# Optimization experiments

Measured on AMD Instinct MI355X. Metric: run time of the kernel, lower is better.

Reference implementation:

```python
import jax, jax.numpy as jnp
import numpy as np

EPS = 1e-08
SLOPE = 0.01  # LeakyReLU default negative_slope
B = 2097152
H = 32

def leaky_relu(x):
    return jnp.where(x >= 0, x, SLOPE * x)

def gram_schmidt(v, w):
    # v, w: [b,3]
    v_on = v / (jnp.linalg.norm(v, axis=-1, keepdims=True) + EPS)
    proj = jnp.sum(w * v_on, axis=-1, keepdims=True) * v_on
    w_orth = w - proj
    w_on = w_orth / (jnp.linalg.norm(w_orth, axis=-1, keepdims=True) + EPS)
    u_on = jnp.cross(v_on, w_on)
    R = jnp.stack((v_on, w_on, u_on), axis=-1)  # [b,3,3]
    v_local = jnp.einsum('bji,bj->bi', R, v)    # R^T @ v
    w_local = jnp.einsum('bji,bj->bi', R, w)
    return R, v_local, w_local

def setup_inputs() -> dict:
    key = jax.random.key(0)
    ks = jax.random.split(key, 12)
    std = 0.0001  # init_weights() normal std
    return {
        'v': jax.random.normal(ks[0], (B, 3), jnp.float32),
        'w': jax.random.normal(ks[1], (B, 3), jnp.float32),
        'W1': jax.random.normal(ks[2], (H, 3), jnp.float32) * std,
        'b1': jax.random.normal(ks[3], (H,), jnp.float32) * std,
        'W2': jax.random.normal(ks[4], (H, H), jnp.float32) * std,
        'b2': jax.random.normal(ks[5], (H,), jnp.float32) * std,
        'Wd1': jax.random.normal(ks[6], (H, H), jnp.float32) * std,
        'bd1': jax.random.normal(ks[7], (H,), jnp.float32) * std,
        'Wd2': jax.random.normal(ks[8], (3, H), jnp.float32) * std,
        'bd2': jax.random.normal(ks[9], (3,), jnp.float32) * std,
        'bias': jnp.array([[0.0, 0.0, -9.81]], jnp.float32),
    }

def reference(v, w, W1, b1, W2, b2, Wd1, bd1, Wd2, bd2, bias):
    shapes = v.shape
    b = shapes[0]
    v = v.reshape(b, 3)
    w = w.reshape(b, 3)
    R, v_local, w_local = gram_schmidt(v, w)
    feat = jnp.concatenate([v_local[..., :1], w_local[..., :2]], axis=-1)  # [b,3]
    h1 = leaky_relu(feat @ W1.T + b1)           # [b,H]
    h = leaky_relu(h1 @ W2.T + b2) * h1         # [b,H]
    y = leaky_relu(h @ Wd1.T + bd1) @ Wd2.T + bd2  # [b,3]
    y = jnp.einsum('bij,bj->bi', R, y) + bias
    return y.reshape(shapes)
```

## Files before the change

### kernel.cpp

```cpp
#include <hip/hip_runtime.h>

typedef __attribute__((ext_vector_type(8))) short short8;
typedef __attribute__((ext_vector_type(4))) float f32x4;
typedef __attribute__((ext_vector_type(4))) unsigned int u32x4;
typedef __attribute__((ext_vector_type(2))) unsigned long long u64x2;

static __device__ __forceinline__ unsigned int fbits(float f) {
    union { float f; unsigned int u; } v; v.f = f; return v.u;
}
static __device__ __forceinline__ float bitsf(unsigned int u) {
    union { float f; unsigned int u; } v; v.u = u; return v.f;
}
static __device__ __forceinline__ unsigned int pkbf(float lo, float hi) {
    return __builtin_amdgcn_perm(fbits(hi), fbits(lo), 0x07060302u);
}
static __device__ __forceinline__ float bflo(unsigned int u) { return bitsf(u << 16); }
static __device__ __forceinline__ float bfhi(unsigned int u) { return bitsf(u & 0xFFFF0000u); }
static __device__ __forceinline__ float leaky(float x) { return fmaxf(x, 0.01f * x); }
static __device__ __forceinline__ float rsqrt_nr(float x) {
    const float r = __builtin_amdgcn_rsqf(x);
    return r * (1.5f - (0.5f * x) * (r * r));
}


__global__ __launch_bounds__(256, 4) void aero_mfma(
    const float* __restrict__ vin, const float* __restrict__ win,
    const float* __restrict__ gW1, const float* __restrict__ gb1,
    const float* __restrict__ gW2, const float* __restrict__ gb2,
    const float* __restrict__ gWd1, const float* __restrict__ gbd1,
    const float* __restrict__ gWd2, const float* __restrict__ gbd2,
    const float* __restrict__ gbias,
    float* __restrict__ out, int nrows)
{
    __shared__ unsigned long long hbuf[256 * 9];
    unsigned int* const h32 = (unsigned int*)hbuf;

    const int tid = threadIdx.x;
    int row = blockIdx.x * 256 + tid;
    if (row >= nrows) row = nrows - 1;

    const int i15   = tid & 15;
    const int quad  = (tid >> 4) & 3;
    const int wbase = tid & 192;

    unsigned int bw2[2][4], bwd1[2][4];
    float b2v[2], bd1v[2];
    #pragma unroll
    for (int u = 0; u < 2; ++u) {
        const int n = u * 16 + i15;
        const float* p2 = gW2  + n * 32 + 4 * quad;
        const float* p3 = gWd1 + n * 32 + 4 * quad;
        #pragma unroll
        for (int j = 0; j < 4; ++j) {
            bw2[u][j]  = pkbf(p2[j], p2[j + 16]);
            bwd1[u][j] = pkbf(p3[j], p3[j + 16]);
        }
        b2v[u]  = gb2[n];
        bd1v[u] = gbd1[n];
    }

    const float v0 = vin[3 * row + 0], v1 = vin[3 * row + 1], v2 = vin[3 * row + 2];
    const float w0 = win[3 * row + 0], w1 = win[3 * row + 1], w2 = win[3 * row + 2];

    const float sv  = v0 * v0 + v1 * v1 + v2 * v2;
    const float rnv = rsqrt_nr(sv);
    const float a0 = v0 * rnv, a1 = v1 * rnv, a2 = v2 * rnv;
    const float proj = w0 * a0 + w1 * a1 + w2 * a2;
    const float o0 = w0 - proj * a0, o1 = w1 - proj * a1, o2 = w2 - proj * a2;
    const float sw  = o0 * o0 + o1 * o1 + o2 * o2;
    const float rnw = rsqrt_nr(sw);
    const float c0 = o0 * rnw, c1 = o1 * rnw, c2 = o2 * rnw;
    const float u0 = a1 * c2 - a2 * c1;
    const float u1 = a2 * c0 - a0 * c2;
    const float u2 = a0 * c1 - a1 * c0;

    const float f0 = sv * rnv;
    const float f1 = proj;
    const float f2 = sw * rnw;

    float h1[32];
    #pragma unroll
    for (int j = 0; j < 32; ++j) {
        float acc = gb1[j];
        acc = fmaf(gW1[3 * j + 0], f0, acc);
        acc = fmaf(gW1[3 * j + 1], f1, acc);
        acc = fmaf(gW1[3 * j + 2], f2, acc);
        h1[j] = leaky(acc);
    }

    {
        unsigned long long* dst = hbuf + tid * 9;
        #pragma unroll
        for (int c2 = 0; c2 < 8; ++c2) {
            const unsigned int lo = pkbf(h1[2 * c2],     h1[2 * c2 + 16]);
            const unsigned int hi = pkbf(h1[2 * c2 + 1], h1[2 * c2 + 17]);
            dst[c2] = (unsigned long long)lo | ((unsigned long long)hi << 32);
        }
    }

    __syncthreads();
    {
        const short8 bf0 = __builtin_bit_cast(short8, (u32x4){bw2[0][0], bw2[0][1], bw2[0][2], bw2[0][3]});
        const short8 bf1 = __builtin_bit_cast(short8, (u32x4){bw2[1][0], bw2[1][1], bw2[1][2], bw2[1][3]});
        const f32x4 cb0 = {b2v[0], b2v[0], b2v[0], b2v[0]};
        const f32x4 cb1 = {b2v[1], b2v[1], b2v[1], b2v[1]};
        #pragma unroll
        for (int t = 0; t < 4; ++t) {
            const int ra = wbase + 16 * t + i15;
            u64x2 av;
            av.x = hbuf[ra * 9 + 2 * quad];
            av.y = hbuf[ra * 9 + 2 * quad + 1];
            const short8 af = __builtin_bit_cast(short8, av);
            const f32x4 acc0 = __builtin_amdgcn_mfma_f32_16x16x32_bf16(af, bf0, cb0, 0, 0, 0);
            const f32x4 acc1 = __builtin_amdgcn_mfma_f32_16x16x32_bf16(af, bf1, cb1, 0, 0, 0);
            const int zr = wbase + 16 * t + 4 * quad;
            #pragma unroll
            for (int r = 0; r < 4; ++r) {
                const unsigned int g = h32[(zr + r) * 18 + i15];
                h32[(zr + r) * 18 + i15] =
                    pkbf(leaky(acc0[r]) * bflo(g), leaky(acc1[r]) * bfhi(g));
            }
        }
    }

    __syncthreads();
    {
        const short8 bf0 = __builtin_bit_cast(short8, (u32x4){bwd1[0][0], bwd1[0][1], bwd1[0][2], bwd1[0][3]});
        const short8 bf1 = __builtin_bit_cast(short8, (u32x4){bwd1[1][0], bwd1[1][1], bwd1[1][2], bwd1[1][3]});
        const f32x4 cb0 = {bd1v[0], bd1v[0], bd1v[0], bd1v[0]};
        const f32x4 cb1 = {bd1v[1], bd1v[1], bd1v[1], bd1v[1]};
        #pragma unroll
        for (int t = 0; t < 4; ++t) {
            const int ra = wbase + 16 * t + i15;
            u64x2 av;
            av.x = hbuf[ra * 9 + 2 * quad];
            av.y = hbuf[ra * 9 + 2 * quad + 1];
            const short8 af = __builtin_bit_cast(short8, av);
            const f32x4 acc0 = __builtin_amdgcn_mfma_f32_16x16x32_bf16(af, bf0, cb0, 0, 0, 0);
            const f32x4 acc1 = __builtin_amdgcn_mfma_f32_16x16x32_bf16(af, bf1, cb1, 0, 0, 0);
            const int zr = wbase + 16 * t + 4 * quad;
            #pragma unroll
            for (int r = 0; r < 4; ++r)
                h32[(zr + r) * 18 + i15] = pkbf(acc0[r], acc1[r]);
        }
    }

    __syncthreads();
    {
        const unsigned long long* src = hbuf + tid * 9;
        float h3[32];
        #pragma unroll
        for (int c2 = 0; c2 < 8; ++c2) {
            const unsigned long long zz = src[c2];
            const unsigned int ulo = (unsigned int)zz;
            const unsigned int uhi = (unsigned int)(zz >> 32);
            h3[2 * c2]      = leaky(bflo(ulo));
            h3[2 * c2 + 16] = leaky(bfhi(ulo));
            h3[2 * c2 + 1]  = leaky(bflo(uhi));
            h3[2 * c2 + 17] = leaky(bfhi(uhi));
        }

        float y0 = gbd2[0], y1 = gbd2[1], y2 = gbd2[2];
        #pragma unroll
        for (int k = 0; k < 32; ++k) {
            y0 = fmaf(gWd2[0 * 32 + k], h3[k], y0);
            y1 = fmaf(gWd2[1 * 32 + k], h3[k], y1);
            y2 = fmaf(gWd2[2 * 32 + k], h3[k], y2);
        }

        out[3 * row + 0] = fmaf(a0, y0, fmaf(c0, y1, fmaf(u0, y2, gbias[0])));
        out[3 * row + 1] = fmaf(a1, y0, fmaf(c1, y1, fmaf(u1, y2, gbias[1])));
        out[3 * row + 2] = fmaf(a2, y0, fmaf(c2, y1, fmaf(u2, y2, gbias[2])));
    }
}

extern "C" void kernel_launch(void* const* d_in, const int* in_sizes, int n_in,
                              void* d_out, int out_size, void* d_ws, size_t ws_size,
                              hipStream_t stream) {
    const float* v    = (const float*)d_in[0];
    const float* w    = (const float*)d_in[1];
    const float* W1   = (const float*)d_in[2];
    const float* b1   = (const float*)d_in[3];
    const float* W2   = (const float*)d_in[4];
    const float* b2   = (const float*)d_in[5];
    const float* Wd1  = (const float*)d_in[6];
    const float* bd1  = (const float*)d_in[7];
    const float* Wd2  = (const float*)d_in[8];
    const float* bd2  = (const float*)d_in[9];
    const float* bias = (const float*)d_in[10];

    const int nrows = in_sizes[0] / 3;
    dim3 block(256);
    dim3 grid((nrows + 255) / 256);
    hipLaunchKernelGGL(aero_mfma, grid, block, 0, stream,
                       v, w, W1, b1, W2, b2, Wd1, bd1, Wd2, bd2, bias,
                       (float*)d_out, nrows);
}
```

Before: 141.4 us.

## Use single-wave blocks and packed FP32 math for the scalar MLP layers

Shrinks the block from 256 to 64 threads so each block is one wavefront, which turns the block-wide barriers into single-wave syncs and shrinks LDS per block. The first layer, the final Wd2 projection and the leaky activations are rewritten with inline-asm v_pk_mul/v_pk_fma/v_pk_add on f32x2 pairs using scalar weight operands, halving the VALU instruction count for those parts. The inline asm forces scalar register operands for weights and may constrain scheduling. Launch bounds of (64,4) may also change register allocation, and 4x more blocks adds scheduling overhead.

Result: slower. 144.7 us (+2.4%).

```diff
diff --git a/kernel.cpp b/kernel.cpp
--- a/kernel.cpp
+++ b/kernel.cpp
@@ -2,6 +2,7 @@
 
 typedef __attribute__((ext_vector_type(8))) short short8;
 typedef __attribute__((ext_vector_type(4))) float f32x4;
+typedef __attribute__((ext_vector_type(2))) float f32x2;
 typedef __attribute__((ext_vector_type(4))) unsigned int u32x4;
 typedef __attribute__((ext_vector_type(2))) unsigned long long u64x2;
 
@@ -22,8 +23,25 @@
     return r * (1.5f - (0.5f * x) * (r * r));
 }
 
-
-__global__ __launch_bounds__(256, 4) void aero_mfma(
+static __device__ __forceinline__ f32x2 pk_mul_s(f32x2 s, f32x2 v) {
+    f32x2 d; asm("v_pk_mul_f32 %0, %1, %2" : "=v"(d) : "s"(s), "v"(v)); return d;
+}
+static __device__ __forceinline__ f32x2 pk_fma_s(f32x2 s, f32x2 v, f32x2 c) {
+    f32x2 d; asm("v_pk_fma_f32 %0, %1, %2, %3" : "=v"(d) : "s"(s), "v"(v), "v"(c)); return d;
+}
+static __device__ __forceinline__ f32x2 pk_add_s(f32x2 s, f32x2 v) {
+    f32x2 d; asm("v_pk_add_f32 %0, %1, %2" : "=v"(d) : "s"(s), "v"(v)); return d;
+}
+static __device__ __forceinline__ f32x2 pk_mul_v(f32x2 a, f32x2 b) {
+    f32x2 d; asm("v_pk_mul_f32 %0, %1, %2" : "=v"(d) : "v"(a), "v"(b)); return d;
+}
+static __device__ __forceinline__ f32x2 leaky2(f32x2 x, f32x2 c001) {
+    const f32x2 m = pk_mul_v(x, c001);
+    f32x2 r; r.x = fmaxf(x.x, m.x); r.y = fmaxf(x.y, m.y); return r;
+}
+
+
+__global__ __launch_bounds__(64, 4) void aero_mfma(
     const float* __restrict__ vin, const float* __restrict__ win,
     const float* __restrict__ gW1, const float* __restrict__ gb1,
     const float* __restrict__ gW2, const float* __restrict__ gb2,
@@ -32,16 +50,15 @@
     const float* __restrict__ gbias,
     float* __restrict__ out, int nrows)
 {
-    __shared__ unsigned long long hbuf[256 * 9];
+    __shared__ unsigned long long hbuf[64 * 9];
     unsigned int* const h32 = (unsigned int*)hbuf;
 
     const int tid = threadIdx.x;
-    int row = blockIdx.x * 256 + tid;
+    int row = blockIdx.x * 64 + tid;
     if (row >= nrows) row = nrows - 1;
 
-    const int i15   = tid & 15;
-    const int quad  = (tid >> 4) & 3;
-    const int wbase = tid & 192;
+    const int i15  = tid & 15;
+    const int quad = (tid >> 4) & 3;
 
     unsigned int bw2[2][4], bwd1[2][4];
     float b2v[2], bd1v[2];
@@ -78,22 +95,30 @@
     const float f1 = proj;
     const float f2 = sw * rnw;
 
-    float h1[32];
-    #pragma unroll
-    for (int j = 0; j < 32; ++j) {
-        float acc = gb1[j];
-        acc = fmaf(gW1[3 * j + 0], f0, acc);
-        acc = fmaf(gW1[3 * j + 1], f1, acc);
-        acc = fmaf(gW1[3 * j + 2], f2, acc);
-        h1[j] = leaky(acc);
+    const f32x2 c001 = {0.01f, 0.01f};
+    f32x2 h1p[16];
+    {
+        const f32x2 fv0 = {f0, f0}, fv1 = {f1, f1}, fv2 = {f2, f2};
+        #pragma unroll
+        for (int j = 0; j < 16; ++j) {
+            const f32x2 wp0 = {gW1[3 * j + 0], gW1[3 * (j + 16) + 0]};
+            const f32x2 wp1 = {gW1[3 * j + 1], gW1[3 * (j + 16) + 1]};
+            const f32x2 wp2 = {gW1[3 * j + 2], gW1[3 * (j + 16) + 2]};
+            const f32x2 bb  = {gb1[j], gb1[j + 16]};
+            f32x2 acc = pk_mul_s(wp0, fv0);
+            acc = pk_fma_s(wp1, fv1, acc);
+            acc = pk_fma_s(wp2, fv2, acc);
+            acc = pk_add_s(bb, acc);
+            h1p[j] = leaky2(acc, c001);
+        }
     }
 
     {
         unsigned long long* dst = hbuf + tid * 9;
         #pragma unroll
         for (int c2 = 0; c2 < 8; ++c2) {
-            const unsigned int lo = pkbf(h1[2 * c2],     h1[2 * c2 + 16]);
-            const unsigned int hi = pkbf(h1[2 * c2 + 1], h1[2 * c2 + 17]);
+            const unsigned int lo = pkbf(h1p[2 * c2].x,     h1p[2 * c2].y);
+            const unsigned int hi = pkbf(h1p[2 * c2 + 1].x, h1p[2 * c2 + 1].y);
             dst[c2] = (unsigned long long)lo | ((unsigned long long)hi << 32);
         }
     }
@@ -106,14 +131,14 @@
         const f32x4 cb1 = {b2v[1], b2v[1], b2v[1], b2v[1]};
         #pragma unroll
         for (int t = 0; t < 4; ++t) {
-            const int ra = wbase + 16 * t + i15;
+            const int ra = 16 * t + i15;
             u64x2 av;
             av.x = hbuf[ra * 9 + 2 * quad];
             av.y = hbuf[ra * 9 + 2 * quad + 1];
             const short8 af = __builtin_bit_cast(short8, av);
             const f32x4 acc0 = __builtin_amdgcn_mfma_f32_16x16x32_bf16(af, bf0, cb0, 0, 0, 0);
             const f32x4 acc1 = __builtin_amdgcn_mfma_f32_16x16x32_bf16(af, bf1, cb1, 0, 0, 0);
-            const int zr = wbase + 16 * t + 4 * quad;
+            const int zr = 16 * t + 4 * quad;
             #pragma unroll
             for (int r = 0; r < 4; ++r) {
                 const unsigned int g = h32[(zr + r) * 18 + i15];
@@ -131,14 +156,14 @@
         const f32x4 cb1 = {bd1v[1], bd1v[1], bd1v[1], bd1v[1]};
         #pragma unroll
         for (int t = 0; t < 4; ++t) {
-            const int ra = wbase + 16 * t + i15;
+            const int ra = 16 * t + i15;
             u64x2 av;
             av.x = hbuf[ra * 9 + 2 * quad];
             av.y = hbuf[ra * 9 + 2 * quad + 1];
             const short8 af = __builtin_bit_cast(short8, av);
             const f32x4 acc0 = __builtin_amdgcn_mfma_f32_16x16x32_bf16(af, bf0, cb0, 0, 0, 0);
             const f32x4 acc1 = __builtin_amdgcn_mfma_f32_16x16x32_bf16(af, bf1, cb1, 0, 0, 0);
-            const int zr = wbase + 16 * t + 4 * quad;
+            const int zr = 16 * t + 4 * quad;
             #pragma unroll
             for (int r = 0; r < 4; ++r)
                 h32[(zr + r) * 18 + i15] = pkbf(acc0[r], acc1[r]);
@@ -148,29 +173,35 @@
     __syncthreads();
     {
         const unsigned long long* src = hbuf + tid * 9;
-        float h3[32];
+        f32x2 he[8], ho[8];
         #pragma unroll
         for (int c2 = 0; c2 < 8; ++c2) {
             const unsigned long long zz = src[c2];
             const unsigned int ulo = (unsigned int)zz;
             const unsigned int uhi = (unsigned int)(zz >> 32);
-            h3[2 * c2]      = leaky(bflo(ulo));
-            h3[2 * c2 + 16] = leaky(bfhi(ulo));
-            h3[2 * c2 + 1]  = leaky(bflo(uhi));
-            h3[2 * c2 + 17] = leaky(bfhi(uhi));
-        }
-
-        float y0 = gbd2[0], y1 = gbd2[1], y2 = gbd2[2];
-        #pragma unroll
-        for (int k = 0; k < 32; ++k) {
-            y0 = fmaf(gWd2[0 * 32 + k], h3[k], y0);
-            y1 = fmaf(gWd2[1 * 32 + k], h3[k], y1);
-            y2 = fmaf(gWd2[2 * 32 + k], h3[k], y2);
-        }
-
-        out[3 * row + 0] = fmaf(a0, y0, fmaf(c0, y1, fmaf(u0, y2, gbias[0])));
-        out[3 * row + 1] = fmaf(a1, y0, fmaf(c1, y1, fmaf(u1, y2, gbias[1])));
-        out[3 * row + 2] = fmaf(a2, y0, fmaf(c2, y1, fmaf(u2, y2, gbias[2])));
+            f32x2 e; e.x = bflo(ulo); e.y = bflo(uhi);
+            f32x2 o; o.x = bfhi(ulo); o.y = bfhi(uhi);
+            he[c2] = leaky2(e, c001);
+            ho[c2] = leaky2(o, c001);
+        }
+
+        float y[3];
+        #pragma unroll
+        for (int j = 0; j < 3; ++j) {
+            const float* wr = gWd2 + j * 32;
+            f32x2 acc = pk_mul_s((f32x2){wr[0], wr[1]}, he[0]);
+            #pragma unroll
+            for (int c2 = 1; c2 < 8; ++c2)
+                acc = pk_fma_s((f32x2){wr[2 * c2], wr[2 * c2 + 1]}, he[c2], acc);
+            #pragma unroll
+            for (int c2 = 0; c2 < 8; ++c2)
+                acc = pk_fma_s((f32x2){wr[16 + 2 * c2], wr[16 + 2 * c2 + 1]}, ho[c2], acc);
+            y[j] = acc.x + acc.y + gbd2[j];
+        }
+
+        out[3 * row + 0] = fmaf(a0, y[0], fmaf(c0, y[1], fmaf(u0, y[2], gbias[0])));
+        out[3 * row + 1] = fmaf(a1, y[0], fmaf(c1, y[1], fmaf(u1, y[2], gbias[1])));
+        out[3 * row + 2] = fmaf(a2, y[0], fmaf(c2, y[1], fmaf(u2, y[2], gbias[2])));
     }
 }
 
@@ -190,8 +221,8 @@
     const float* bias = (const float*)d_in[10];
 
     const int nrows = in_sizes[0] / 3;
-    dim3 block(256);
-    dim3 grid((nrows + 255) / 256);
+    dim3 block(64);
+    dim3 grid((nrows + 63) / 64);
     hipLaunchKernelGGL(aero_mfma, grid, block, 0, stream,
                        v, w, W1, b1, W2, b2, Wd1, bd1, Wd2, bd2, bias,
                        (float*)d_out, nrows);
```

## Chain MLP layers in registers via transposed MFMA, removing LDS round trips

Applied to the files above, without the earlier changes.

The layers are reformulated so the weights become the MFMA A operand and the activations the B operand. The output of the second layer then lands directly in the fragment layout needed for the third layer, so the intermediate activations stay in registers and two LDS round trips and two barriers are removed. The final 32->3 projection is done in registers with packed FP32 math plus cross-lane shuffles, where before each thread ran a 96-FMA loop. The first layer also uses packed FP32 ops via inline asm. The cost is extra shuffles and per-tile select logic, plus reliance on correct SGPR operand constraints in the inline asm.

Result: no change. 140.5 us (-0.6%).

```diff
diff --git a/kernel.cpp b/kernel.cpp
--- a/kernel.cpp
+++ b/kernel.cpp
@@ -2,8 +2,8 @@
 
 typedef __attribute__((ext_vector_type(8))) short short8;
 typedef __attribute__((ext_vector_type(4))) float f32x4;
+typedef __attribute__((ext_vector_type(2))) float f32x2;
 typedef __attribute__((ext_vector_type(4))) unsigned int u32x4;
-typedef __attribute__((ext_vector_type(2))) unsigned long long u64x2;
 
 static __device__ __forceinline__ unsigned int fbits(float f) {
     union { float f; unsigned int u; } v; v.f = f; return v.u;
@@ -20,6 +20,25 @@
 static __device__ __forceinline__ float rsqrt_nr(float x) {
     const float r = __builtin_amdgcn_rsqf(x);
     return r * (1.5f - (0.5f * x) * (r * r));
+}
+static __device__ __forceinline__ f32x2 pk_mul_s(f32x2 s, f32x2 v) {
+    f32x2 d; asm("v_pk_mul_f32 %0, %1, %2" : "=v"(d) : "s"(s), "v"(v)); return d;
+}
+static __device__ __forceinline__ f32x2 pk_fma_s(f32x2 s, f32x2 v, f32x2 c) {
+    f32x2 d; asm("v_pk_fma_f32 %0, %1, %2, %3" : "=v"(d) : "s"(s), "v"(v), "v"(c)); return d;
+}
+static __device__ __forceinline__ f32x2 pk_add_s(f32x2 s, f32x2 v) {
+    f32x2 d; asm("v_pk_add_f32 %0, %1, %2" : "=v"(d) : "s"(s), "v"(v)); return d;
+}
+static __device__ __forceinline__ f32x2 pk_mul_v(f32x2 a, f32x2 b) {
+    f32x2 d; asm("v_pk_mul_f32 %0, %1, %2" : "=v"(d) : "v"(a), "v"(b)); return d;
+}
+static __device__ __forceinline__ f32x2 pk_fma_v(f32x2 a, f32x2 b, f32x2 c) {
+    f32x2 d; asm("v_pk_fma_f32 %0, %1, %2, %3" : "=v"(d) : "v"(a), "v"(b), "v"(c)); return d;
+}
+static __device__ __forceinline__ f32x2 leaky2(f32x2 x, f32x2 c001) {
+    const f32x2 m = pk_mul_v(x, c001);
+    f32x2 r; r.x = fmaxf(x.x, m.x); r.y = fmaxf(x.y, m.y); return r;
 }
 
 
@@ -32,32 +51,49 @@
     const float* __restrict__ gbias,
     float* __restrict__ out, int nrows)
 {
-    __shared__ unsigned long long hbuf[256 * 9];
-    unsigned int* const h32 = (unsigned int*)hbuf;
-
-    const int tid = threadIdx.x;
+    __shared__ unsigned int h1lds[256 * 20];
+
+    const int tid  = threadIdx.x;
     int row = blockIdx.x * 256 + tid;
     if (row >= nrows) row = nrows - 1;
 
     const int i15   = tid & 15;
     const int quad  = (tid >> 4) & 3;
     const int wbase = tid & 192;
-
-    unsigned int bw2[2][4], bwd1[2][4];
-    float b2v[2], bd1v[2];
+    const int ko    = 4 * quad;
+
+    unsigned int aW2lo[4], aW2hi[4], aWd1lo[4], aWd1hi[4];
+    {
+        const float* p;
+        p = gW2 + i15 * 32 + ko;
+        { f32x4 xa = *(const f32x4*)p, xb = *(const f32x4*)(p + 16);
+          #pragma unroll
+          for (int j = 0; j < 4; ++j) aW2lo[j] = pkbf(xa[j], xb[j]); }
+        p = gW2 + (16 + i15) * 32 + ko;
+        { f32x4 xa = *(const f32x4*)p, xb = *(const f32x4*)(p + 16);
+          #pragma unroll
+          for (int j = 0; j < 4; ++j) aW2hi[j] = pkbf(xa[j], xb[j]); }
+        p = gWd1 + i15 * 32 + ko;
+        { f32x4 xa = *(const f32x4*)p, xb = *(const f32x4*)(p + 16);
+          #pragma unroll
+          for (int j = 0; j < 4; ++j) aWd1lo[j] = pkbf(xa[j], xb[j]); }
+        p = gWd1 + (16 + i15) * 32 + ko;
+        { f32x4 xa = *(const f32x4*)p, xb = *(const f32x4*)(p + 16);
+          #pragma unroll
+          for (int j = 0; j < 4; ++j) aWd1hi[j] = pkbf(xa[j], xb[j]); }
+    }
+    f32x2 wd2p[3][4];
     #pragma unroll
-    for (int u = 0; u < 2; ++u) {
-        const int n = u * 16 + i15;
-        const float* p2 = gW2  + n * 32 + 4 * quad;
-        const float* p3 = gWd1 + n * 32 + 4 * quad;
-        #pragma unroll
-        for (int j = 0; j < 4; ++j) {
-            bw2[u][j]  = pkbf(p2[j], p2[j + 16]);
-            bwd1[u][j] = pkbf(p3[j], p3[j + 16]);
-        }
-        b2v[u]  = gb2[n];
-        bd1v[u] = gbd1[n];
-    }
+    for (int f = 0; f < 3; ++f) {
+        const f32x4 xa = *(const f32x4*)(gWd2 + f * 32 + ko);
+        const f32x4 xb = *(const f32x4*)(gWd2 + f * 32 + ko + 16);
+        #pragma unroll
+        for (int r = 0; r < 4; ++r) { wd2p[f][r].x = xa[r]; wd2p[f][r].y = xb[r]; }
+    }
+    const f32x4 cb2lo  = *(const f32x4*)(gb2  + ko);
+    const f32x4 cb2hi  = *(const f32x4*)(gb2  + 16 + ko);
+    const f32x4 cbd1lo = *(const f32x4*)(gbd1 + ko);
+    const f32x4 cbd1hi = *(const f32x4*)(gbd1 + 16 + ko);
 
     const float v0 = vin[3 * row + 0], v1 = vin[3 * row + 1], v2 = vin[3 * row + 2];
     const float w0 = win[3 * row + 0], w1 = win[3 * row + 1], w2 = win[3 * row + 2];
@@ -74,104 +110,83 @@
     const float u1 = a2 * c0 - a0 * c2;
     const float u2 = a0 * c1 - a1 * c0;
 
-    const float f0 = sv * rnv;
-    const float f1 = proj;
-    const float f2 = sw * rnw;
-
-    float h1[32];
+    const float f0 = sv * rnv, f1 = proj, f2 = sw * rnw;
+
+    const f32x2 c001 = {0.01f, 0.01f};
+    {
+        const f32x2 fv0 = {f0, f0}, fv1 = {f1, f1}, fv2 = {f2, f2};
+        unsigned int hp[16];
+        #pragma unroll
+        for (int j = 0; j < 16; ++j) {
+            const f32x2 wp0 = {gW1[3 * j + 0], gW1[3 * (j + 16) + 0]};
+            const f32x2 wp1 = {gW1[3 * j + 1], gW1[3 * (j + 16) + 1]};
+            const f32x2 wp2 = {gW1[3 * j + 2], gW1[3 * (j + 16) + 2]};
+            const f32x2 bb  = {gb1[j], gb1[j + 16]};
+            f32x2 acc = pk_mul_s(wp0, fv0);
+            acc = pk_fma_s(wp1, fv1, acc);
+            acc = pk_fma_s(wp2, fv2, acc);
+            acc = pk_add_s(bb, acc);
+            const f32x2 h = leaky2(acc, c001);
+            hp[j] = pkbf(h.x, h.y);
+        }
+        unsigned int* dst = &h1lds[tid * 20];
+        *(u32x4*)(dst +  0) = (u32x4){hp[0],  hp[1],  hp[2],  hp[3]};
+        *(u32x4*)(dst +  4) = (u32x4){hp[4],  hp[5],  hp[6],  hp[7]};
+        *(u32x4*)(dst +  8) = (u32x4){hp[8],  hp[9],  hp[10], hp[11]};
+        *(u32x4*)(dst + 12) = (u32x4){hp[12], hp[13], hp[14], hp[15]};
+    }
+    __syncthreads();
+
+    float y0 = 0.f, y1 = 0.f, y2 = 0.f;
     #pragma unroll
-    for (int j = 0; j < 32; ++j) {
-        float acc = gb1[j];
-        acc = fmaf(gW1[3 * j + 0], f0, acc);
-        acc = fmaf(gW1[3 * j + 1], f1, acc);
-        acc = fmaf(gW1[3 * j + 2], f2, acc);
-        h1[j] = leaky(acc);
-    }
-
-    {
-        unsigned long long* dst = hbuf + tid * 9;
-        #pragma unroll
-        for (int c2 = 0; c2 < 8; ++c2) {
-            const unsigned int lo = pkbf(h1[2 * c2],     h1[2 * c2 + 16]);
-            const unsigned int hi = pkbf(h1[2 * c2 + 1], h1[2 * c2 + 17]);
-            dst[c2] = (unsigned long long)lo | ((unsigned long long)hi << 32);
+    for (int t = 0; t < 4; ++t) {
+        const u32x4 bfr = *(const u32x4*)(&h1lds[(wbase + 16 * t + i15) * 20 + ko]);
+        const short8 bfrag = __builtin_bit_cast(short8, bfr);
+
+        const f32x4 accA = __builtin_amdgcn_mfma_f32_16x16x32_bf16(
+            __builtin_bit_cast(short8, (u32x4){aW2lo[0], aW2lo[1], aW2lo[2], aW2lo[3]}),
+            bfrag, cb2lo, 0, 0, 0);
+        const f32x4 accB = __builtin_amdgcn_mfma_f32_16x16x32_bf16(
+            __builtin_bit_cast(short8, (u32x4){aW2hi[0], aW2hi[1], aW2hi[2], aW2hi[3]}),
+            bfrag, cb2hi, 0, 0, 0);
+
+        u32x4 h2u;
+        #pragma unroll
+        for (int r = 0; r < 4; ++r)
+            h2u[r] = pkbf(leaky(accA[r]) * bflo(bfr[r]),
+                          leaky(accB[r]) * bfhi(bfr[r]));
+        const short8 h2frag = __builtin_bit_cast(short8, h2u);
+
+        const f32x4 accC = __builtin_amdgcn_mfma_f32_16x16x32_bf16(
+            __builtin_bit_cast(short8, (u32x4){aWd1lo[0], aWd1lo[1], aWd1lo[2], aWd1lo[3]}),
+            h2frag, cbd1lo, 0, 0, 0);
+        const f32x4 accD = __builtin_amdgcn_mfma_f32_16x16x32_bf16(
+            __builtin_bit_cast(short8, (u32x4){aWd1hi[0], aWd1hi[1], aWd1hi[2], aWd1hi[3]}),
+            h2frag, cbd1hi, 0, 0, 0);
+
+        f32x2 h3p[4];
+        #pragma unroll
+        for (int r = 0; r < 4; ++r) { h3p[r].x = leaky(accC[r]); h3p[r].y = leaky(accD[r]); }
+        f32x2 P0 = pk_mul_v(wd2p[0][0], h3p[0]);
+        f32x2 P1 = pk_mul_v(wd2p[1][0], h3p[0]);
+        f32x2 P2 = pk_mul_v(wd2p[2][0], h3p[0]);
+        #pragma unroll
+        for (int r = 1; r < 4; ++r) {
+            P0 = pk_fma_v(wd2p[0][r], h3p[r], P0);
+            P1 = pk_fma_v(wd2p[1][r], h3p[r], P1);
+            P2 = pk_fma_v(wd2p[2][r], h3p[r], P2);
         }
-    }
-
-    __syncthreads();
-    {
-        const short8 bf0 = __builtin_bit_cast(short8, (u32x4){bw2[0][0], bw2[0][1], bw2[0][2], bw2[0][3]});
-        const short8 bf1 = __builtin_bit_cast(short8, (u32x4){bw2[1][0], bw2[1][1], bw2[1][2], bw2[1][3]});
-        const f32x4 cb0 = {b2v[0], b2v[0], b2v[0], b2v[0]};
-        const f32x4 cb1 = {b2v[1], b2v[1], b2v[1], b2v[1]};
-        #pragma unroll
-        for (int t = 0; t < 4; ++t) {
-            const int ra = wbase + 16 * t + i15;
-            u64x2 av;
-            av.x = hbuf[ra * 9 + 2 * quad];
-            av.y = hbuf[ra * 9 + 2 * quad + 1];
-            const short8 af = __builtin_bit_cast(short8, av);
-            const f32x4 acc0 = __builtin_amdgcn_mfma_f32_16x16x32_bf16(af, bf0, cb0, 0, 0, 0);
-            const f32x4 acc1 = __builtin_amdgcn_mfma_f32_16x16x32_bf16(af, bf1, cb1, 0, 0, 0);
-            const int zr = wbase + 16 * t + 4 * quad;
-            #pragma unroll
-            for (int r = 0; r < 4; ++r) {
-                const unsigned int g = h32[(zr + r) * 18 + i15];
-                h32[(zr + r) * 18 + i15] =
-                    pkbf(leaky(acc0[r]) * bflo(g), leaky(acc1[r]) * bfhi(g));
-            }
-        }
-    }
-
-    __syncthreads();
-    {
-        const short8 bf0 = __builtin_bit_cast(short8, (u32x4){bwd1[0][0], bwd1[0][1], bwd1[0][2], bwd1[0][3]});
-        const short8 bf1 = __builtin_bit_cast(short8, (u32x4){bwd1[1][0], bwd1[1][1], bwd1[1][2], bwd1[1][3]});
-        const f32x4 cb0 = {bd1v[0], bd1v[0], bd1v[0], bd1v[0]};
-        const f32x4 cb1 = {bd1v[1], bd1v[1], bd1v[1], bd1v[1]};
-        #pragma unroll
-        for (int t = 0; t < 4; ++t) {
-            const int ra = wbase + 16 * t + i15;
-            u64x2 av;
-            av.x = hbuf[ra * 9 + 2 * quad];
-            av.y = hbuf[ra * 9 + 2 * quad + 1];
-            const short8 af = __builtin_bit_cast(short8, av);
-            const f32x4 acc0 = __builtin_amdgcn_mfma_f32_16x16x32_bf16(af, bf0, cb0, 0, 0, 0);
-            const f32x4 acc1 = __builtin_amdgcn_mfma_f32_16x16x32_bf16(af, bf1, cb1, 0, 0, 0);
-            const int zr = wbase + 16 * t + 4 * quad;
-            #pragma unroll
-            for (int r = 0; r < 4; ++r)
-                h32[(zr + r) * 18 + i15] = pkbf(acc0[r], acc1[r]);
-        }
-    }
-
-    __syncthreads();
-    {
-        const unsigned long long* src = hbuf + tid * 9;
-        float h3[32];
-        #pragma unroll
-        for (int c2 = 0; c2 < 8; ++c2) {
-            const unsigned long long zz = src[c2];
-            const unsigned int ulo = (unsigned int)zz;
-            const unsigned int uhi = (unsigned int)(zz >> 32);
-            h3[2 * c2]      = leaky(bflo(ulo));
-            h3[2 * c2 + 16] = leaky(bfhi(ulo));
-            h3[2 * c2 + 1]  = leaky(bflo(uhi));
-            h3[2 * c2 + 17] = leaky(bfhi(uhi));
-        }
-
-        float y0 = gbd2[0], y1 = gbd2[1], y2 = gbd2[2];
-        #pragma unroll
-        for (int k = 0; k < 32; ++k) {
-            y0 = fmaf(gWd2[0 * 32 + k], h3[k], y0);
-            y1 = fmaf(gWd2[1 * 32 + k], h3[k], y1);
-            y2 = fmaf(gWd2[2 * 32 + k], h3[k], y2);
-        }
-
-        out[3 * row + 0] = fmaf(a0, y0, fmaf(c0, y1, fmaf(u0, y2, gbias[0])));
-        out[3 * row + 1] = fmaf(a1, y0, fmaf(c1, y1, fmaf(u1, y2, gbias[1])));
-        out[3 * row + 2] = fmaf(a2, y0, fmaf(c2, y1, fmaf(u2, y2, gbias[2])));
-    }
+        float s0 = P0.x + P0.y, s1 = P1.x + P1.y, s2 = P2.x + P2.y;
+        s0 += __shfl_xor(s0, 16); s0 += __shfl_xor(s0, 32);
+        s1 += __shfl_xor(s1, 16); s1 += __shfl_xor(s1, 32);
+        s2 += __shfl_xor(s2, 16); s2 += __shfl_xor(s2, 32);
+        if (quad == t) { y0 = s0; y1 = s1; y2 = s2; }
+    }
+    y0 += gbd2[0]; y1 += gbd2[1]; y2 += gbd2[2];
+
+    out[3 * row + 0] = fmaf(a0, y0, fmaf(c0, y1, fmaf(u0, y2, gbias[0])));
+    out[3 * row + 1] = fmaf(a1, y0, fmaf(c1, y1, fmaf(u1, y2, gbias[1])));
+    out[3 * row + 2] = fmaf(a2, y0, fmaf(c2, y1, fmaf(u2, y2, gbias[2])));
 }
 
 extern "C" void kernel_launch(void* const* d_in, const int* in_sizes, int n_in,
```
